# Kernel optimization log

Hardware: AMD Instinct MI355X
Metric: run time of the kernel (lower is better)

The kernel has to match this reference:

```python
import jax, jax.numpy as jnp
import numpy as np

TEMPERATURE = 1.0

def setup_inputs() -> dict:
    key = jax.random.key(0)
    k1, k2 = jax.random.split(key)
    B, I, O = 256, 1024, 1024
    x = jax.random.normal(k1, (B, I), dtype=jnp.float32)
    # mimic TruncatedNormal(stddev=1/sqrt(input_size)) init
    w = jax.random.normal(k2, (I, O), dtype=jnp.float32) * (1.0 / np.sqrt(I))
    b = jnp.zeros((O,), dtype=jnp.float32)
    return {"x": x, "w": w, "b": b}

def reference(x, w, b):
    # z: [B, I, O] outer product per sample
    z = jnp.einsum('bi,io->bio', x, w)
    n = x.shape[-1]
    # per-output-neuron temperature softmax over the input dim I
    s = jax.nn.softmax(jnp.abs(z) / TEMPERATURE, axis=1)
    out = n * jnp.sum(z * s, axis=1)  # [B, O]
    return out + b
```

## Files before the change

kernel.cpp:

```cpp
#include <hip/hip_runtime.h>

#define BDIM 256
#define IDIM 1024
#define ODIM 1024

#define NW 8
#define QLEN 128
#define NO 16
#define NPAIR (QLEN / 2)

typedef float v2f __attribute__((ext_vector_type(2)));

#if __has_builtin(__builtin_amdgcn_exp2f)
#define FAST_EXP2(v) __builtin_amdgcn_exp2f(v)
#else
#define FAST_EXP2(v) exp2f(v)
#endif

__global__ __launch_bounds__(256)
void prep_kernel(const float* __restrict__ x, const float* __restrict__ w,
                 float* __restrict__ wS, float* __restrict__ xT) {
  __shared__ float lt[64][65];
  const int tid = threadIdx.x;
  const float LOG2E = 1.4426950408889634f;
  const int t = blockIdx.x;
  if (t < 256) {
    const int i0 = (t >> 4) * 64, o0 = (t & 15) * 64;
#pragma unroll
    for (int k = 0; k < 16; ++k) {
      int idx = tid + k * 256, r = idx >> 6, c = idx & 63;
      lt[r][c] = LOG2E * w[(size_t)(i0 + r) * ODIM + o0 + c];
    }
    __syncthreads();
#pragma unroll
    for (int k = 0; k < 16; ++k) {
      int idx = tid + k * 256, ol = idx >> 6, il = idx & 63;
      int gi = i0 + il, go = o0 + ol;
      int e = gi >> 7, ip = gi & 127;
      wS[(size_t)e * (ODIM * QLEN) + (size_t)go * QLEN + ip] = lt[il][ol];
    }
  } else {
    const int t2 = t - 256;
    const int i0 = (t2 >> 2) * 64, b0 = (t2 & 3) * 64;
#pragma unroll
    for (int k = 0; k < 16; ++k) {
      int idx = tid + k * 256, r = idx >> 6, c = idx & 63;
      lt[r][c] = x[(size_t)(b0 + r) * IDIM + i0 + c];
    }
    __syncthreads();
#pragma unroll
    for (int k = 0; k < 16; ++k) {
      int idx = tid + k * 256, il = idx >> 6, bl = idx & 63;
      xT[(size_t)(i0 + il) * BDIM + b0 + bl] = lt[bl][il];
    }
  }
}

__global__ __launch_bounds__(512, 2)
void stl_main(const float* __restrict__ xT, const float* __restrict__ wS,
              const float* __restrict__ bias, float* __restrict__ out) {
  __shared__ float ps[NW][64][2 * NO];

  const int tx = threadIdx.x;
  const int ty = threadIdx.y;
  const int o0 = blockIdx.x * NO;
  const int b0 = blockIdx.y * 64;
  const int tyu = __builtin_amdgcn_readfirstlane(ty);
  const int qbase = tyu * QLEN;

  v2f xv[NPAIR];
#pragma unroll
  for (int u = 0; u < NPAIR; ++u) {
    xv[u].x = xT[(size_t)(qbase + 2 * u) * BDIM + b0 + tx];
    xv[u].y = xT[(size_t)(qbase + 2 * u + 1) * BDIM + b0 + tx];
  }

  const float* wrow = wS + (size_t)tyu * (ODIM * QLEN) + (size_t)o0 * QLEN;

  for (int o = 0; o < NO; ++o) {
    const float* wr = wrow + (size_t)o * QLEN;
    v2f accn = {0.f, 0.f}, accd = {0.f, 0.f};
#pragma unroll
    for (int k = 0; k < NPAIR; ++k) {
      v2f sw;
      sw.x = wr[2 * k];
      sw.y = wr[2 * k + 1];
      v2f p = xv[k] * sw;
      v2f t;
      t.x = FAST_EXP2(__builtin_fabsf(p.x));
      t.y = FAST_EXP2(__builtin_fabsf(p.y));
      accn += p * t;
      accd += t;
    }
    v2f res;
    res.x = accn.x + accn.y;
    res.y = accd.x + accd.y;
    *(v2f*)&ps[ty][tx][2 * o] = res;
  }
  __syncthreads();

  const int tid = ty * 64 + tx;
  const int b = tid >> 3;
  const int op = (tid & 7) * 2;
  float n0 = 0.f, d0 = 0.f, n1 = 0.f, d1 = 0.f;
#pragma unroll
  for (int wv = 0; wv < NW; ++wv) {
    float4 a = *(const float4*)&ps[wv][b][2 * op];
    n0 += a.x; d0 += a.y; n1 += a.z; d1 += a.w;
  }
  const float LN2 = 0.6931471805599453f;
  const float scale = (float)IDIM * LN2;
  float2 r;
  r.x = scale * n0 / d0 + bias[o0 + op];
  r.y = scale * n1 / d1 + bias[o0 + op + 1];
  *(float2*)&out[(size_t)(b0 + b) * ODIM + o0 + op] = r;
}

#define TILE_OL 2
#define TILE_O (64 * TILE_OL)
#define TILE_B 4
#define FQLEN (IDIM / NW)
#define CHUNK 8
#define NCHUNK (FQLEN / CHUNK)

typedef float v4f __attribute__((ext_vector_type(4)));

__global__ __launch_bounds__(512, 4)
void stl_old(const float* __restrict__ x, const float* __restrict__ w,
             const float* __restrict__ bias, float* __restrict__ out) {
  __shared__ float xs[TILE_B][IDIM];
  __shared__ float ps[NW][64][16];

  const int tx = threadIdx.x, ty = threadIdx.y;
  const int tid = ty * 64 + tx;
  const int o0 = blockIdx.x * TILE_O;
  const int b0 = blockIdx.y * TILE_B;
  const float LOG2E = 1.4426950408889634f;

#pragma unroll
  for (int k = 0; k < 2; ++k) {
    int f = tid + k * 512, row = f >> 8, col = f & 255;
    float4 v = ((const float4*)(x + (size_t)(b0 + row) * IDIM))[col];
    v.x *= LOG2E; v.y *= LOG2E; v.z *= LOG2E; v.w *= LOG2E;
    ((float4*)(&xs[row][0]))[col] = v;
  }
  __syncthreads();

  const int qbase = ty * FQLEN;
  const float* wp = w + (size_t)qbase * ODIM + o0 + tx;

  v2f an[TILE_OL][TILE_B], ad[TILE_OL][TILE_B];
#pragma unroll
  for (int s = 0; s < TILE_OL; ++s)
#pragma unroll
    for (int r = 0; r < TILE_B; ++r) { an[s][r] = (v2f){0.f, 0.f}; ad[s][r] = (v2f){0.f, 0.f}; }

  v2f wA0[CHUNK / 2], wA1[CHUNK / 2], wB0[CHUNK / 2], wB1[CHUNK / 2];

#define WLOADF(d0_, d1_, cc)                                              \
  {                                                                       \
    const float* wq = wp + (size_t)((cc) * CHUNK) * ODIM;                 \
    _Pragma("unroll")                                                     \
    for (int u = 0; u < CHUNK / 2; ++u) {                                 \
      d0_[u].x = wq[(size_t)(2 * u) * ODIM];                              \
      d0_[u].y = wq[(size_t)(2 * u + 1) * ODIM];                          \
      d1_[u].x = wq[(size_t)(2 * u) * ODIM + 64];                         \
      d1_[u].y = wq[(size_t)(2 * u + 1) * ODIM + 64];                     \
    }                                                                     \
  }

#define ROWPF(acc_n, acc_d, xpair, wpair)                                 \
  {                                                                       \
    v2f p = (xpair) * (wpair);                                            \
    v2f t;                                                                \
    t.x = FAST_EXP2(__builtin_fabsf(p.x));                                \
    t.y = FAST_EXP2(__builtin_fabsf(p.y));                                \
    acc_n += p * t;                                                       \
    acc_d += t;                                                           \
  }

#define LOF(xq) __builtin_shufflevector(xq, xq, 0, 1)
#define HIF(xq) __builtin_shufflevector(xq, xq, 2, 3)

#define COMPUTEF(wc0, wc1, cc)                                            \
  {                                                                       \
    const int jb = qbase + (cc) * CHUNK;                                  \
    _Pragma("unroll")                                                     \
    for (int h = 0; h < 2; ++h) {                                         \
      v4f xq[TILE_B];                                                     \
      _Pragma("unroll")                                                   \
      for (int r = 0; r < TILE_B; ++r)                                    \
        xq[r] = *(const v4f*)(&xs[r][jb + h * 4]);                        \
      _Pragma("unroll")                                                   \
      for (int r = 0; r < TILE_B; ++r) {                                  \
        ROWPF(an[0][r], ad[0][r], LOF(xq[r]), wc0[h * 2])                 \
        ROWPF(an[0][r], ad[0][r], HIF(xq[r]), wc0[h * 2 + 1])             \
        ROWPF(an[1][r], ad[1][r], LOF(xq[r]), wc1[h * 2])                 \
        ROWPF(an[1][r], ad[1][r], HIF(xq[r]), wc1[h * 2 + 1])             \
      }                                                                   \
    }                                                                     \
  }

  WLOADF(wA0, wA1, 0)
  for (int c = 0; c < NCHUNK; c += 2) {
    WLOADF(wB0, wB1, c + 1)
    COMPUTEF(wA0, wA1, c)
    WLOADF(wA0, wA1, (c + 2) & (NCHUNK - 1))
    COMPUTEF(wB0, wB1, c + 1)
  }

#pragma unroll
  for (int s = 0; s < TILE_OL; ++s) {
    *(float4*)(&ps[ty][tx][s * 8 + 0]) =
        make_float4(an[s][0].x + an[s][0].y, an[s][1].x + an[s][1].y,
                    an[s][2].x + an[s][2].y, an[s][3].x + an[s][3].y);
    *(float4*)(&ps[ty][tx][s * 8 + 4]) =
        make_float4(ad[s][0].x + ad[s][0].y, ad[s][1].x + ad[s][1].y,
                    ad[s][2].x + ad[s][2].y, ad[s][3].x + ad[s][3].y);
  }
  __syncthreads();

  if (ty == 0) {
    const float LN2 = 0.6931471805599453f;
    const float scale = (float)IDIM * LN2;
#pragma unroll
    for (int s = 0; s < TILE_OL; ++s) {
      float n[4] = {0, 0, 0, 0}, d[4] = {0, 0, 0, 0};
#pragma unroll
      for (int q = 0; q < NW; ++q) {
        float4 a = *(const float4*)(&ps[q][tx][s * 8 + 0]);
        float4 b2 = *(const float4*)(&ps[q][tx][s * 8 + 4]);
        n[0] += a.x; n[1] += a.y; n[2] += a.z; n[3] += a.w;
        d[0] += b2.x; d[1] += b2.y; d[2] += b2.z; d[3] += b2.w;
      }
      const int o = o0 + tx + s * 64;
      const float bo = bias[o];
#pragma unroll
      for (int r = 0; r < 4; ++r)
        out[(size_t)(b0 + r) * ODIM + o] = scale * n[r] / d[r] + bo;
    }
  }
}

extern "C" void kernel_launch(void* const* d_in, const int* in_sizes, int n_in,
                              void* d_out, int out_size, void* d_ws, size_t ws_size,
                              hipStream_t stream) {
  const float* x = (const float*)d_in[0];
  const float* w = (const float*)d_in[1];
  const float* b = (const float*)d_in[2];
  float* out = (float*)d_out;

  const size_t wS_bytes = (size_t)NW * ODIM * QLEN * sizeof(float);
  const size_t xT_bytes = (size_t)IDIM * BDIM * sizeof(float);

  if (ws_size >= wS_bytes + xT_bytes) {
    float* wS = (float*)d_ws;
    float* xT = (float*)((char*)d_ws + wS_bytes);
    prep_kernel<<<320, 256, 0, stream>>>(x, w, wS, xT);
    dim3 grid(ODIM / NO, BDIM / 64);
    dim3 block(64, NW);
    stl_main<<<grid, block, 0, stream>>>(xT, wS, b, out);
  } else {
    dim3 grid(ODIM / TILE_O, BDIM / TILE_B);
    dim3 block(64, NW);
    stl_old<<<grid, block, 0, stream>>>(x, w, b, out);
  }
}
```

Measured before the change: 97.96 us.

## Split input dim across 16 waves with 8 outputs per block and finer prep tiles

Reworks the main kernel to split the input dimension into 16 slices of 64 (1024-thread blocks) and process 8 outputs per block, doubling the grid width. The aim is more parallelism and shorter per-wave register footprints. The prep kernel moves to 32x32 tiles with 1280 blocks, and the weight row pointer is forced into scalar registers via readfirstlane. The partial-sum layout in shared memory is transposed so writes are per-lane contiguous. Half the threads now idle during the final reduction, and there is more cross-wave reduction work.

Result: slower. 116.7 us (+19.1%).

```diff
diff --git a/kernel.cpp b/kernel.cpp
--- a/kernel.cpp
+++ b/kernel.cpp
@@ -4,12 +4,13 @@
 #define IDIM 1024
 #define ODIM 1024
 
-#define NW 8
-#define QLEN 128
-#define NO 16
-#define NPAIR (QLEN / 2)
+#define NW2 16
+#define QL2 64
+#define NP2 32
+#define NO2 8
 
 typedef float v2f __attribute__((ext_vector_type(2)));
+typedef float v4f __attribute__((ext_vector_type(4)));
 
 #if __has_builtin(__builtin_amdgcn_exp2f)
 #define FAST_EXP2(v) __builtin_amdgcn_exp2f(v)
@@ -17,71 +18,77 @@
 #define FAST_EXP2(v) exp2f(v)
 #endif
 
+__device__ __forceinline__ const float* uptr(const float* p) {
+  unsigned long long v = (unsigned long long)p;
+  unsigned lo = __builtin_amdgcn_readfirstlane((unsigned)v);
+  unsigned hi = __builtin_amdgcn_readfirstlane((unsigned)(v >> 32));
+  return (const float*)(((unsigned long long)hi << 32) | lo);
+}
+
 __global__ __launch_bounds__(256)
-void prep_kernel(const float* __restrict__ x, const float* __restrict__ w,
-                 float* __restrict__ wS, float* __restrict__ xT) {
-  __shared__ float lt[64][65];
+void prep2(const float* __restrict__ x, const float* __restrict__ w,
+           float* __restrict__ wS, float* __restrict__ xT) {
+  __shared__ float lt[32][33];
   const int tid = threadIdx.x;
   const float LOG2E = 1.4426950408889634f;
   const int t = blockIdx.x;
-  if (t < 256) {
-    const int i0 = (t >> 4) * 64, o0 = (t & 15) * 64;
-#pragma unroll
-    for (int k = 0; k < 16; ++k) {
-      int idx = tid + k * 256, r = idx >> 6, c = idx & 63;
+  if (t < 1024) {
+    const int i0 = (t >> 5) * 32, o0 = (t & 31) * 32;
+#pragma unroll
+    for (int k = 0; k < 4; ++k) {
+      int idx = tid + k * 256, r = idx >> 5, c = idx & 31;
       lt[r][c] = LOG2E * w[(size_t)(i0 + r) * ODIM + o0 + c];
     }
     __syncthreads();
-#pragma unroll
-    for (int k = 0; k < 16; ++k) {
-      int idx = tid + k * 256, ol = idx >> 6, il = idx & 63;
-      int gi = i0 + il, go = o0 + ol;
-      int e = gi >> 7, ip = gi & 127;
-      wS[(size_t)e * (ODIM * QLEN) + (size_t)go * QLEN + ip] = lt[il][ol];
+    const int e = i0 >> 6, ib = i0 & 63;
+#pragma unroll
+    for (int k = 0; k < 4; ++k) {
+      int idx = tid + k * 256, orr = idx >> 5, ir = idx & 31;
+      wS[(size_t)e * (ODIM * QL2) + (size_t)(o0 + orr) * QL2 + ib + ir] = lt[ir][orr];
     }
   } else {
-    const int t2 = t - 256;
-    const int i0 = (t2 >> 2) * 64, b0 = (t2 & 3) * 64;
-#pragma unroll
-    for (int k = 0; k < 16; ++k) {
-      int idx = tid + k * 256, r = idx >> 6, c = idx & 63;
+    const int t2 = t - 1024;
+    const int b0 = (t2 >> 5) * 32, i0 = (t2 & 31) * 32;
+#pragma unroll
+    for (int k = 0; k < 4; ++k) {
+      int idx = tid + k * 256, r = idx >> 5, c = idx & 31;
       lt[r][c] = x[(size_t)(b0 + r) * IDIM + i0 + c];
     }
     __syncthreads();
 #pragma unroll
-    for (int k = 0; k < 16; ++k) {
-      int idx = tid + k * 256, il = idx >> 6, bl = idx & 63;
+    for (int k = 0; k < 4; ++k) {
+      int idx = tid + k * 256, il = idx >> 5, bl = idx & 31;
       xT[(size_t)(i0 + il) * BDIM + b0 + bl] = lt[bl][il];
     }
   }
 }
 
-__global__ __launch_bounds__(512, 2)
+__global__ __launch_bounds__(1024, 4)
 void stl_main(const float* __restrict__ xT, const float* __restrict__ wS,
               const float* __restrict__ bias, float* __restrict__ out) {
-  __shared__ float ps[NW][64][2 * NO];
+  __shared__ float ps[NW2][2 * NO2][64];
 
   const int tx = threadIdx.x;
   const int ty = threadIdx.y;
-  const int o0 = blockIdx.x * NO;
+  const int o0 = blockIdx.x * NO2;
   const int b0 = blockIdx.y * 64;
   const int tyu = __builtin_amdgcn_readfirstlane(ty);
-  const int qbase = tyu * QLEN;
-
-  v2f xv[NPAIR];
-#pragma unroll
-  for (int u = 0; u < NPAIR; ++u) {
+  const int qbase = tyu * QL2;
+
+  v2f xv[NP2];
+#pragma unroll
+  for (int u = 0; u < NP2; ++u) {
     xv[u].x = xT[(size_t)(qbase + 2 * u) * BDIM + b0 + tx];
     xv[u].y = xT[(size_t)(qbase + 2 * u + 1) * BDIM + b0 + tx];
   }
 
-  const float* wrow = wS + (size_t)tyu * (ODIM * QLEN) + (size_t)o0 * QLEN;
-
-  for (int o = 0; o < NO; ++o) {
-    const float* wr = wrow + (size_t)o * QLEN;
-    v2f accn = {0.f, 0.f}, accd = {0.f, 0.f};
-#pragma unroll
-    for (int k = 0; k < NPAIR; ++k) {
+  const float* wrow = uptr(wS + (size_t)tyu * (ODIM * QL2) + (size_t)o0 * QL2);
+
+  for (int o = 0; o < NO2; ++o) {
+    const float* wr = wrow + (size_t)o * QL2;
+    v2f an = {0.f, 0.f}, ad = {0.f, 0.f};
+#pragma unroll
+    for (int k = 0; k < NP2; ++k) {
       v2f sw;
       sw.x = wr[2 * k];
       sw.y = wr[2 * k + 1];
@@ -89,41 +96,37 @@
       v2f t;
       t.x = FAST_EXP2(__builtin_fabsf(p.x));
       t.y = FAST_EXP2(__builtin_fabsf(p.y));
-      accn += p * t;
-      accd += t;
-    }
-    v2f res;
-    res.x = accn.x + accn.y;
-    res.y = accd.x + accd.y;
-    *(v2f*)&ps[ty][tx][2 * o] = res;
+      an += p * t;
+      ad += t;
+    }
+    ps[ty][2 * o][tx] = an.x + an.y;
+    ps[ty][2 * o + 1][tx] = ad.x + ad.y;
   }
   __syncthreads();
 
   const int tid = ty * 64 + tx;
-  const int b = tid >> 3;
-  const int op = (tid & 7) * 2;
-  float n0 = 0.f, d0 = 0.f, n1 = 0.f, d1 = 0.f;
-#pragma unroll
-  for (int wv = 0; wv < NW; ++wv) {
-    float4 a = *(const float4*)&ps[wv][b][2 * op];
-    n0 += a.x; d0 += a.y; n1 += a.z; d1 += a.w;
-  }
-  const float LN2 = 0.6931471805599453f;
-  const float scale = (float)IDIM * LN2;
-  float2 r;
-  r.x = scale * n0 / d0 + bias[o0 + op];
-  r.y = scale * n1 / d1 + bias[o0 + op + 1];
-  *(float2*)&out[(size_t)(b0 + b) * ODIM + o0 + op] = r;
-}
-
+  if (tid < 512) {
+    const int b = tid >> 3;
+    const int op = tid & 7;
+    float n = 0.f, d = 0.f;
+#pragma unroll
+    for (int wv = 0; wv < NW2; ++wv) {
+      n += ps[wv][2 * op][b];
+      d += ps[wv][2 * op + 1][b];
+    }
+    const float LN2 = 0.6931471805599453f;
+    const float scale = (float)IDIM * LN2;
+    out[(size_t)(b0 + b) * ODIM + o0 + op] = scale * n / d + bias[o0 + op];
+  }
+}
+
+#define NW 8
 #define TILE_OL 2
 #define TILE_O (64 * TILE_OL)
 #define TILE_B 4
 #define FQLEN (IDIM / NW)
 #define CHUNK 8
 #define NCHUNK (FQLEN / CHUNK)
-
-typedef float v4f __attribute__((ext_vector_type(4)));
 
 __global__ __launch_bounds__(512, 4)
 void stl_old(const float* __restrict__ x, const float* __restrict__ w,
@@ -250,15 +253,15 @@
   const float* b = (const float*)d_in[2];
   float* out = (float*)d_out;
 
-  const size_t wS_bytes = (size_t)NW * ODIM * QLEN * sizeof(float);
+  const size_t wS_bytes = (size_t)NW2 * ODIM * QL2 * sizeof(float);
   const size_t xT_bytes = (size_t)IDIM * BDIM * sizeof(float);
 
   if (ws_size >= wS_bytes + xT_bytes) {
     float* wS = (float*)d_ws;
     float* xT = (float*)((char*)d_ws + wS_bytes);
-    prep_kernel<<<320, 256, 0, stream>>>(x, w, wS, xT);
-    dim3 grid(ODIM / NO, BDIM / 64);
-    dim3 block(64, NW);
+    prep2<<<1280, 256, 0, stream>>>(x, w, wS, xT);
+    dim3 grid(ODIM / NO2, BDIM / 64);
+    dim3 block(64, NW2);
     stl_main<<<grid, block, 0, stream>>>(xT, wS, b, out);
   } else {
     dim3 grid(ODIM / TILE_O, BDIM / TILE_B);
```
